# Performance work log

Measured on AMD Instinct MI355X. Metric: run time of the kernel, lower is better.

## Reference

```python
import jax, jax.numpy as jnp
import numpy as np

L, N, E = 2048, 2, 512
H = 8
HD = E // H
FF = 2048
NLAYERS = 2
EPS = 1e-5


def setup_inputs() -> dict:
    key = jax.random.key(0)
    ks = jax.random.split(key, 8)
    s = 0.02
    return {
        "src": jax.random.normal(ks[0], (L, N, E), jnp.float32),
        # packed qkv projection, torch Linear convention: y = x @ W.T + b
        "in_proj_w": jax.random.normal(ks[1], (NLAYERS, 3 * E, E), jnp.float32) * s,
        "in_proj_b": jnp.zeros((NLAYERS, 3 * E), jnp.float32),
        "out_proj_w": jax.random.normal(ks[2], (NLAYERS, E, E), jnp.float32) * s,
        "out_proj_b": jnp.zeros((NLAYERS, E), jnp.float32),
        "lin1_w": jax.random.normal(ks[3], (NLAYERS, FF, E), jnp.float32) * s,
        "lin1_b": jnp.zeros((NLAYERS, FF), jnp.float32),
        "lin2_w": jax.random.normal(ks[4], (NLAYERS, E, FF), jnp.float32) * s,
        "lin2_b": jnp.zeros((NLAYERS, E), jnp.float32),
        "ln1_g": jnp.ones((NLAYERS, E), jnp.float32),
        "ln1_b": jnp.zeros((NLAYERS, E), jnp.float32),
        "ln2_g": jnp.ones((NLAYERS, E), jnp.float32),
        "ln2_b": jnp.zeros((NLAYERS, E), jnp.float32),
    }


def _layer_norm(x, g, b):
    mu = jnp.mean(x, axis=-1, keepdims=True)
    var = jnp.mean(jnp.square(x - mu), axis=-1, keepdims=True)
    return (x - mu) * jax.lax.rsqrt(var + EPS) * g + b


def _mha(x, w_qkv, b_qkv, w_o, b_o):
    # x: [L, N, E] (seq-first, as in torch multi_head_attention_forward)
    qkv = jnp.einsum('lne,fe->lnf', x, w_qkv) + b_qkv  # [L, N, 3E]
    q, k, v = jnp.split(qkv, 3, axis=-1)
    q = q.reshape(L, N, H, HD) * (1.0 / np.sqrt(HD))  # torch scales q pre-bmm
    k = k.reshape(L, N, H, HD)
    v = v.reshape(L, N, H, HD)
    scores = jnp.einsum('lnhd,snhd->nhls', q, k)  # [N, H, L, S] -- O(L*S) matrix
    attn = jax.nn.softmax(scores, axis=-1)
    o = jnp.einsum('nhls,snhd->lnhd', attn, v).reshape(L, N, E)
    return jnp.einsum('lne,fe->lnf', o, w_o) + b_o


def reference(src, in_proj_w, in_proj_b, out_proj_w, out_proj_b,
              lin1_w, lin1_b, lin2_w, lin2_b, ln1_g, ln1_b, ln2_g, ln2_b):
    x = src
    for i in range(NLAYERS):  # fixed small layer count
        a = _mha(x, in_proj_w[i], in_proj_b[i], out_proj_w[i], out_proj_b[i])
        x = _layer_norm(x + a, ln1_g[i], ln1_b[i])  # post-norm (torch default)
        h = jax.nn.relu(jnp.einsum('lne,fe->lnf', x, lin1_w[i]) + lin1_b[i])
        f = jnp.einsum('lnf,ef->lne', h, lin2_w[i]) + lin2_b[i]
        x = _layer_norm(x + f, ln2_g[i], ln2_b[i])
    return x
```

## Files before the change

### kernel.cpp

```cpp
#include <hip/hip_runtime.h>
#include <hip/hip_bf16.h>

using bf16 = __hip_bfloat16;
typedef __bf16 bf16x8 __attribute__((ext_vector_type(8)));
typedef float f32x4 __attribute__((ext_vector_type(4)));

#define MFMA(a, b, c) __builtin_amdgcn_mfma_f32_16x16x32_bf16(a, b, c, 0, 0, 0)

constexpr int L = 2048, N = 2, E = 512, H = 8, HD = 64, FF = 2048;
constexpr int T = L * N;

__global__ void detect_dtype(const unsigned int* __restrict__ g,
                             int* __restrict__ flag) {
  if (threadIdx.x == 0 && blockIdx.x == 0)
    *flag = (g[0] != 0x3F800000u) ? 1 : 0;
}

__global__ __launch_bounds__(256) void cvt_to_bf16(
    const void* __restrict__ in, bf16* __restrict__ out, int n,
    const int* __restrict__ flag) {
  int i = (blockIdx.x * 256 + threadIdx.x) * 8;
  if (i >= n) return;
  if (*flag) {
    *(uint4*)&out[i] = *(const uint4*)&((const bf16*)in)[i];
  } else {
    float4 a = *(const float4*)&((const float*)in)[i];
    float4 b = *(const float4*)&((const float*)in)[i + 4];
    bf16 o8[8] = {__float2bfloat16(a.x), __float2bfloat16(a.y),
                  __float2bfloat16(a.z), __float2bfloat16(a.w),
                  __float2bfloat16(b.x), __float2bfloat16(b.y),
                  __float2bfloat16(b.z), __float2bfloat16(b.w)};
    *(uint4*)&out[i] = *(const uint4*)o8;
  }
}

__global__ __launch_bounds__(256) void cvt_to_f32(
    const void* __restrict__ in, float* __restrict__ out, int n,
    const int* __restrict__ flag) {
  int i = blockIdx.x * 256 + threadIdx.x;
  if (i >= n) return;
  out[i] = (*flag) ? __bfloat162float(((const bf16*)in)[i])
                   : ((const float*)in)[i];
}

__device__ __forceinline__ void gload16(const bf16* g, bf16* l) {
  __builtin_amdgcn_global_load_lds(
      (const __attribute__((address_space(1))) unsigned int*)g,
      (__attribute__((address_space(3))) unsigned int*)l, 16, 0, 0);
}

template <bool RELU>
__global__ __launch_bounds__(256) void gemm128(
    const bf16* __restrict__ A, const bf16* __restrict__ W,
    const float* __restrict__ bias, bf16* __restrict__ C,
    int M, int F, int K) {
  __shared__ __align__(16) bf16 As[2][128 * 32];
  __shared__ __align__(16) bf16 Bs[2][128 * 32];
  const int bm = blockIdx.x, bn = blockIdx.y;
  const int tid = threadIdx.x;
  const int w = tid >> 6, lane = tid & 63;
  const int wr = w >> 1, wc = w & 1;
  const int lhi = lane >> 4, llo = lane & 15;
  f32x4 acc[4][4] = {};

  const bf16 *ap[2], *wp[2];
#pragma unroll
  for (int s = 0; s < 2; ++s) {
    int c = tid + s * 256;
    ap[s] = &A[(size_t)(bm * 128 + (c >> 2)) * K + (c & 3) * 8];
    wp[s] = &W[(size_t)(bn * 128 + (c >> 2)) * K + (c & 3) * 8];
  }
  auto stage = [&](int buf, int k0) {
#pragma unroll
    for (int s = 0; s < 2; ++s) {
      gload16(ap[s] + k0, &As[buf][(tid + s * 256) * 8]);
      gload16(wp[s] + k0, &Bs[buf][(tid + s * 256) * 8]);
    }
  };

  stage(0, 0);
  int cur = 0;
  for (int k0 = 0; k0 < K; k0 += 32) {
    __syncthreads();
    if (k0 + 32 < K) stage(cur ^ 1, k0 + 32);
    bf16x8 af[4], bfr[4];
#pragma unroll
    for (int mi = 0; mi < 4; ++mi)
      af[mi] =
          *(const bf16x8*)&As[cur][(wr * 64 + mi * 16 + llo) * 32 + lhi * 8];
#pragma unroll
    for (int ni = 0; ni < 4; ++ni)
      bfr[ni] =
          *(const bf16x8*)&Bs[cur][(wc * 64 + ni * 16 + llo) * 32 + lhi * 8];
#pragma unroll
    for (int mi = 0; mi < 4; ++mi)
#pragma unroll
      for (int ni = 0; ni < 4; ++ni)
        acc[mi][ni] = MFMA(af[mi], bfr[ni], acc[mi][ni]);
    cur ^= 1;
  }
#pragma unroll
  for (int mi = 0; mi < 4; ++mi) {
#pragma unroll
    for (int ni = 0; ni < 4; ++ni) {
      int col = bn * 128 + wc * 64 + ni * 16 + llo;
      float bv = bias[col];
#pragma unroll
      for (int r = 0; r < 4; ++r) {
        int row = bm * 128 + wr * 64 + mi * 16 + lhi * 4 + r;
        float v = acc[mi][ni][r] + bv;
        if (RELU) v = fmaxf(v, 0.f);
        C[(size_t)row * F + col] = __float2bfloat16(v);
      }
    }
  }
}

template <bool RELU>
__global__ __launch_bounds__(256) void gemm64(
    const bf16* __restrict__ A, const bf16* __restrict__ W,
    const float* __restrict__ bias, bf16* __restrict__ C,
    int M, int F, int K) {
  __shared__ __align__(16) bf16 As[2][64 * 32];
  __shared__ __align__(16) bf16 Bs[2][64 * 32];
  const int bm = blockIdx.x, bn = blockIdx.y;
  const int tid = threadIdx.x;
  const int w = tid >> 6, lane = tid & 63;
  const int wr = w >> 1, wc = w & 1;
  const int lhi = lane >> 4, llo = lane & 15;
  f32x4 acc[2][2] = {};

  const bf16* ap = &A[(size_t)(bm * 64 + (tid >> 2)) * K + (tid & 3) * 8];
  const bf16* wp = &W[(size_t)(bn * 64 + (tid >> 2)) * K + (tid & 3) * 8];
  auto stage = [&](int buf, int k0) {
    gload16(ap + k0, &As[buf][tid * 8]);
    gload16(wp + k0, &Bs[buf][tid * 8]);
  };

  stage(0, 0);
  int cur = 0;
  for (int k0 = 0; k0 < K; k0 += 32) {
    __syncthreads();
    if (k0 + 32 < K) stage(cur ^ 1, k0 + 32);
    bf16x8 af[2], bfr[2];
#pragma unroll
    for (int mi = 0; mi < 2; ++mi)
      af[mi] =
          *(const bf16x8*)&As[cur][(wr * 32 + mi * 16 + llo) * 32 + lhi * 8];
#pragma unroll
    for (int ni = 0; ni < 2; ++ni)
      bfr[ni] =
          *(const bf16x8*)&Bs[cur][(wc * 32 + ni * 16 + llo) * 32 + lhi * 8];
#pragma unroll
    for (int mi = 0; mi < 2; ++mi)
#pragma unroll
      for (int ni = 0; ni < 2; ++ni)
        acc[mi][ni] = MFMA(af[mi], bfr[ni], acc[mi][ni]);
    cur ^= 1;
  }
#pragma unroll
  for (int mi = 0; mi < 2; ++mi) {
#pragma unroll
    for (int ni = 0; ni < 2; ++ni) {
      int col = bn * 64 + wc * 32 + ni * 16 + llo;
      float bv = bias[col];
#pragma unroll
      for (int r = 0; r < 4; ++r) {
        int row = bm * 64 + wr * 32 + mi * 16 + lhi * 4 + r;
        float v = acc[mi][ni][r] + bv;
        if (RELU) v = fmaxf(v, 0.f);
        C[(size_t)row * F + col] = __float2bfloat16(v);
      }
    }
  }
}

__global__ __launch_bounds__(256) void prep_kv(
    const bf16* __restrict__ qkv, bf16* __restrict__ kt,
    bf16* __restrict__ vt) {
  __shared__ __align__(16) bf16 Vl[64 * 72];
  const int blk = blockIdx.x;
  const int kb = blk & 31, nh = blk >> 5;
  const int n = nh >> 3, h = nh & 7;
  const int tid = threadIdx.x;
  bf16* ko = kt + ((size_t)nh * 32 + kb) * 4096;
  bf16* vo = vt + ((size_t)nh * 32 + kb) * 4096;
#pragma unroll
  for (int s = 0; s < 2; ++s) {
    int c = tid + s * 256;
    int jj = c >> 3, g = c & 7;
    size_t t = (size_t)((kb * 64 + jj) * N + n);
    uint4 kk = *(const uint4*)&qkv[t * 1536 + 512 + h * 64 + g * 8];
    *(uint4*)&ko[jj * 64 + ((g ^ (jj & 7)) * 8)] = kk;
    uint4 vv = *(const uint4*)&qkv[t * 1536 + 1024 + h * 64 + g * 8];
    *(uint4*)&Vl[jj * 72 + g * 8] = vv;
  }
  __syncthreads();
#pragma unroll
  for (int s = 0; s < 2; ++s) {
    int c = tid + s * 256;
    int d = c >> 3, gsw = c & 7;
    int g = gsw ^ (d & 7);
    bf16 tmp[8];
#pragma unroll
    for (int e = 0; e < 8; ++e) tmp[e] = Vl[(g * 8 + e) * 72 + d];
    *(uint4*)&vo[d * 64 + gsw * 8] = *(const uint4*)tmp;
  }
}

__global__ __launch_bounds__(256) void attn_split(
    const bf16* __restrict__ qkv, const bf16* __restrict__ kt,
    const bf16* __restrict__ vt, float* __restrict__ opart,
    float* __restrict__ lpart) {
  __shared__ __align__(16) bf16 Kb[2][4096];
  __shared__ __align__(16) bf16 Vb[2][4096];
  __shared__ __align__(16) bf16 Ps[64 * 72];
  const int blk = blockIdx.x;
  const int qb = blk & 31;
  const int nh = (blk >> 5) & 15;
  const int split = blk >> 9;
  const int n = nh >> 3, h = nh & 7;
  const int tid = threadIdx.x;
  const int w = tid >> 6, lane = tid & 63;
  const int lhi = lane >> 4, llo = lane & 15;
  const int kb0 = split * 16, kb1 = kb0 + 16;

#pragma unroll
  for (int s = 0; s < 2; ++s) {
    int c = tid + s * 256;
    int i = c >> 3, dc = c & 7;
    size_t t = (size_t)((qb * 64 + i) * N + n);
    *(uint4*)&Ps[i * 72 + dc * 8] =
        *(const uint4*)&qkv[t * 1536 + h * 64 + dc * 8];
  }
  __syncthreads();
  bf16x8 aq[2];
  aq[0] = *(const bf16x8*)&Ps[(w * 16 + llo) * 72 + 0 + lhi * 8];
  aq[1] = *(const bf16x8*)&Ps[(w * 16 + llo) * 72 + 32 + lhi * 8];

  const bf16* ktile = kt + (size_t)nh * 32 * 4096;
  const bf16* vtile = vt + (size_t)nh * 32 * 4096;
  auto stage = [&](int buf, int kb) {
#pragma unroll
    for (int s = 0; s < 2; ++s) {
      int c = tid + s * 256;
      gload16(ktile + (size_t)kb * 4096 + c * 8, &Kb[buf][c * 8]);
      gload16(vtile + (size_t)kb * 4096 + c * 8, &Vb[buf][c * 8]);
    }
  };
  stage(0, kb0);

  float psum[4] = {0.f, 0.f, 0.f, 0.f};
  f32x4 o[4] = {};
  int cur = 0;

  for (int kb = kb0; kb < kb1; ++kb) {
    __syncthreads();
    if (kb + 1 < kb1) stage(cur ^ 1, kb + 1);

    f32x4 sfr[4] = {};
    __builtin_amdgcn_s_setprio(1);
#pragma unroll
    for (int cb = 0; cb < 4; ++cb) {
      const int row = cb * 16 + llo;
#pragma unroll
      for (int ks = 0; ks < 2; ++ks) {
        bf16x8 b = *(const bf16x8*)&Kb[cur]
            [row * 64 + (((ks * 4 + lhi) ^ (row & 7)) << 3)];
        sfr[cb] = MFMA(aq[ks], b, sfr[cb]);
      }
    }
    __builtin_amdgcn_s_setprio(0);

#pragma unroll
    for (int cb = 0; cb < 4; ++cb) {
#pragma unroll
      for (int r = 0; r < 4; ++r) {
        float p = __expf(sfr[cb][r] * 0.125f);
        psum[r] += p;
        Ps[(w * 16 + lhi * 4 + r) * 72 + cb * 16 + llo] = __float2bfloat16(p);
      }
    }
    asm volatile("" ::: "memory");

    __builtin_amdgcn_s_setprio(1);
#pragma unroll
    for (int cb = 0; cb < 4; ++cb) {
      const int crow = cb * 16 + llo;
#pragma unroll
      for (int ks = 0; ks < 2; ++ks) {
        bf16x8 a =
            *(const bf16x8*)&Ps[(w * 16 + llo) * 72 + ks * 32 + lhi * 8];
        bf16x8 b = *(const bf16x8*)&Vb[cur]
            [crow * 64 + (((ks * 4 + lhi) ^ (crow & 7)) << 3)];
        o[cb] = MFMA(a, b, o[cb]);
      }
    }
    __builtin_amdgcn_s_setprio(0);
    cur ^= 1;
  }

#pragma unroll
  for (int r = 0; r < 4; ++r) {
    float v = psum[r];
#pragma unroll
    for (int d = 1; d < 16; d <<= 1) v += __shfl_xor(v, d);
    psum[r] = v;
  }
#pragma unroll
  for (int cb = 0; cb < 4; ++cb) {
#pragma unroll
    for (int r = 0; r < 4; ++r) {
      int i = w * 16 + lhi * 4 + r;
      int d = cb * 16 + llo;
      size_t t = (size_t)((qb * 64 + i) * N + n);
      opart[((size_t)split * T + t) * E + h * 64 + d] = o[cb][r];
    }
  }
  if (llo == 0) {
#pragma unroll
    for (int r = 0; r < 4; ++r) {
      int i = w * 16 + lhi * 4 + r;
      size_t t = (size_t)((qb * 64 + i) * N + n);
      lpart[(size_t)(split * T + t) * H + h] = psum[r];
    }
  }
}

__global__ __launch_bounds__(256) void attn_merge(
    const float* __restrict__ opart, const float* __restrict__ lpart,
    bf16* __restrict__ atn) {
  int i = (blockIdx.x * 256 + threadIdx.x) * 4;
  if (i >= T * E) return;
  int t = i >> 9;
  int h = (i >> 6) & 7;
  float4 o0 = *(const float4*)&opart[i];
  float4 o1 = *(const float4*)&opart[(size_t)T * E + i];
  float rl = 1.f / (lpart[(size_t)t * H + h] + lpart[(size_t)(T + t) * H + h]);
  bf16 r4[4] = {__float2bfloat16((o0.x + o1.x) * rl),
                __float2bfloat16((o0.y + o1.y) * rl),
                __float2bfloat16((o0.z + o1.z) * rl),
                __float2bfloat16((o0.w + o1.w) * rl)};
  *(uint2*)&atn[i] = *(const uint2*)r4;
}

template <typename OutT>
__global__ __launch_bounds__(256) void add_ln(
    const bf16* __restrict__ res, const bf16* __restrict__ y,
    const float* __restrict__ g, const float* __restrict__ b,
    OutT* __restrict__ out) {
  const int t = blockIdx.x;
  const int tid = threadIdx.x;
  const int w = tid >> 6, lane = tid & 63;
  const int e = tid * 2;
  const size_t base = (size_t)t * E;
  float v0 = __bfloat162float(res[base + e]) + __bfloat162float(y[base + e]);
  float v1 = __bfloat162float(res[base + e + 1]) + __bfloat162float(y[base + e + 1]);
  float s = v0 + v1, q = v0 * v0 + v1 * v1;
#pragma unroll
  for (int d = 1; d < 64; d <<= 1) {
    s += __shfl_xor(s, d);
    q += __shfl_xor(q, d);
  }
  __shared__ float rs[4], rq[4];
  if (lane == 0) { rs[w] = s; rq[w] = q; }
  __syncthreads();
  float S = rs[0] + rs[1] + rs[2] + rs[3];
  float Qq = rq[0] + rq[1] + rq[2] + rq[3];
  float mu = S * (1.f / E);
  float var = Qq * (1.f / E) - mu * mu;
  float rstd = rsqrtf(var + 1e-5f);
  float o0 = (v0 - mu) * rstd * g[e] + b[e];
  float o1 = (v1 - mu) * rstd * g[e + 1] + b[e + 1];
  if constexpr (__is_same(OutT, float)) {
    out[base + e] = o0;
    out[base + e + 1] = o1;
  } else {
    out[base + e] = __float2bfloat16(o0);
    out[base + e + 1] = __float2bfloat16(o1);
  }
}

extern "C" void kernel_launch(void* const* d_in, const int* in_sizes, int n_in,
                              void* d_out, int out_size, void* d_ws,
                              size_t ws_size, hipStream_t stream) {
  int* flag = (int*)d_ws;
  float* pbuf = (float*)((char*)d_ws + 16);
  float* in_b = pbuf;
  float* ob   = in_b + 3072;
  float* l1b  = ob + 1024;
  float* l2b  = l1b + 4096;
  float* ln1g = l2b + 1024;
  float* ln1b = ln1g + 1024;
  float* ln2g = ln1b + 1024;
  float* ln2b = ln2g + 1024;
  bf16* big  = (bf16*)(ln2b + 1024);
  bf16* srcb = big;
  bf16* in_w = srcb + (size_t)T * E;
  bf16* ow   = in_w + (size_t)2 * 1536 * E;
  bf16* l1w  = ow + (size_t)2 * E * E;
  bf16* l2w  = l1w + (size_t)2 * FF * E;
  bf16* qkv  = l2w + (size_t)2 * E * FF;
  bf16* atn  = qkv + (size_t)T * 1536;
  bf16* ybuf = atn + (size_t)T * E;
  bf16* x1   = ybuf + (size_t)T * E;
  bf16* x2   = x1 + (size_t)T * E;
  bf16* hbuf = x2 + (size_t)T * E;
  bf16* ktg  = hbuf + (size_t)T * FF;
  bf16* vtg  = ktg + (size_t)T * E;
  float* opart = (float*)hbuf;
  float* lpart = (float*)ybuf;

  detect_dtype<<<1, 64, 0, stream>>>((const unsigned int*)d_in[9], flag);
  auto cvtb = [&](const void* in, bf16* out, int n) {
    cvt_to_bf16<<<dim3(n / 2048), 256, 0, stream>>>(in, out, n, flag);
  };
  auto cvtf = [&](const void* in, float* out, int n) {
    cvt_to_f32<<<dim3(n / 256), 256, 0, stream>>>(in, out, n, flag);
  };
  cvtb(d_in[0], srcb, T * E);
  cvtb(d_in[1], in_w, 2 * 1536 * E);
  cvtb(d_in[3], ow, 2 * E * E);
  cvtb(d_in[5], l1w, 2 * FF * E);
  cvtb(d_in[7], l2w, 2 * E * FF);
  cvtf(d_in[2], in_b, 3072);
  cvtf(d_in[4], ob, 1024);
  cvtf(d_in[6], l1b, 4096);
  cvtf(d_in[8], l2b, 1024);
  cvtf(d_in[9], ln1g, 1024);
  cvtf(d_in[10], ln1b, 1024);
  cvtf(d_in[11], ln2g, 1024);
  cvtf(d_in[12], ln2b, 1024);

  const bf16* x = srcb;
  for (int i = 0; i < 2; ++i) {
    gemm128<false><<<dim3(T / 128, 1536 / 128), 256, 0, stream>>>(
        x, in_w + (size_t)i * 1536 * E, in_b + i * 1536, qkv, T, 1536, E);
    prep_kv<<<dim3(512), 256, 0, stream>>>(qkv, ktg, vtg);
    attn_split<<<dim3(1024), 256, 0, stream>>>(qkv, ktg, vtg, opart, lpart);
    attn_merge<<<dim3(T * E / 1024), 256, 0, stream>>>(opart, lpart, atn);
    gemm64<false><<<dim3(T / 64, E / 64), 256, 0, stream>>>(
        atn, ow + (size_t)i * E * E, ob + i * E, ybuf, T, E, E);
    add_ln<bf16><<<dim3(T), 256, 0, stream>>>(
        x, ybuf, ln1g + i * E, ln1b + i * E, x1);
    gemm128<true><<<dim3(T / 128, FF / 128), 256, 0, stream>>>(
        x1, l1w + (size_t)i * FF * E, l1b + i * FF, hbuf, T, FF, E);
    gemm64<false><<<dim3(T / 64, E / 64), 256, 0, stream>>>(
        hbuf, l2w + (size_t)i * E * FF, l2b + i * E, ybuf, T, E, FF);
    if (i == 1) {
      add_ln<float><<<dim3(T), 256, 0, stream>>>(
          x1, ybuf, ln2g + i * E, ln2b + i * E, (float*)d_out);
    } else {
      add_ln<bf16><<<dim3(T), 256, 0, stream>>>(
          x1, ybuf, ln2g + i * E, ln2b + i * E, x2);
    }
    x = x2;
  }
}
```

Before: 326.4 us.

## Deepen GEMM pipeline to four stages and split attention four ways with bf16 partials

```diff
diff --git a/kernel.cpp b/kernel.cpp
--- a/kernel.cpp
+++ b/kernel.cpp
@@ -49,124 +49,94 @@
       (__attribute__((address_space(3))) unsigned int*)l, 16, 0, 0);
 }
 
-template <bool RELU>
-__global__ __launch_bounds__(256) void gemm128(
+template <bool RELU, int BN>
+__global__ __launch_bounds__(256) void gemm_pipe(
     const bf16* __restrict__ A, const bf16* __restrict__ W,
     const float* __restrict__ bias, bf16* __restrict__ C,
     int M, int F, int K) {
-  __shared__ __align__(16) bf16 As[2][128 * 32];
-  __shared__ __align__(16) bf16 Bs[2][128 * 32];
+  constexpr int D = 4;
+  constexpr int GB = BN / 64;
+  constexpr int FN = BN / 32;
+  __shared__ __align__(16) bf16 As[D][128 * 32];
+  __shared__ __align__(16) bf16 Bs[D][BN * 32];
   const int bm = blockIdx.x, bn = blockIdx.y;
   const int tid = threadIdx.x;
   const int w = tid >> 6, lane = tid & 63;
   const int wr = w >> 1, wc = w & 1;
   const int lhi = lane >> 4, llo = lane & 15;
-  f32x4 acc[4][4] = {};
-
-  const bf16 *ap[2], *wp[2];
+  f32x4 acc[4][FN] = {};
+
+  const bf16 *ap[2], *wp[GB];
 #pragma unroll
   for (int s = 0; s < 2; ++s) {
     int c = tid + s * 256;
     ap[s] = &A[(size_t)(bm * 128 + (c >> 2)) * K + (c & 3) * 8];
-    wp[s] = &W[(size_t)(bn * 128 + (c >> 2)) * K + (c & 3) * 8];
+  }
+#pragma unroll
+  for (int s = 0; s < GB; ++s) {
+    int c = tid + s * 256;
+    wp[s] = &W[(size_t)(bn * BN + (c >> 2)) * K + (c & 3) * 8];
   }
   auto stage = [&](int buf, int k0) {
 #pragma unroll
-    for (int s = 0; s < 2; ++s) {
+    for (int s = 0; s < 2; ++s)
       gload16(ap[s] + k0, &As[buf][(tid + s * 256) * 8]);
+#pragma unroll
+    for (int s = 0; s < GB; ++s)
       gload16(wp[s] + k0, &Bs[buf][(tid + s * 256) * 8]);
-    }
   };
 
+  const int nsteps = K / 32;
   stage(0, 0);
-  int cur = 0;
-  for (int k0 = 0; k0 < K; k0 += 32) {
-    __syncthreads();
-    if (k0 + 32 < K) stage(cur ^ 1, k0 + 32);
-    bf16x8 af[4], bfr[4];
+  stage(1, 32);
+  stage(2, 64);
+
+  for (int t = 0; t < nsteps; ++t) {
+    const int cur = t & 3;
+    if (t < nsteps - 2) {
+      if constexpr (BN == 128)
+        asm volatile("s_waitcnt vmcnt(8)" ::: "memory");
+      else
+        asm volatile("s_waitcnt vmcnt(6)" ::: "memory");
+    } else if (t == nsteps - 2) {
+      if constexpr (BN == 128)
+        asm volatile("s_waitcnt vmcnt(4)" ::: "memory");
+      else
+        asm volatile("s_waitcnt vmcnt(3)" ::: "memory");
+    } else {
+      asm volatile("s_waitcnt vmcnt(0)" ::: "memory");
+    }
+    __builtin_amdgcn_s_barrier();
+    asm volatile("" ::: "memory");
+    __builtin_amdgcn_sched_barrier(0);
+    if (t + 3 < nsteps) stage((t + 3) & 3, (t + 3) * 32);
+
+    bf16x8 af[4], bfr[FN];
 #pragma unroll
     for (int mi = 0; mi < 4; ++mi)
       af[mi] =
           *(const bf16x8*)&As[cur][(wr * 64 + mi * 16 + llo) * 32 + lhi * 8];
 #pragma unroll
-    for (int ni = 0; ni < 4; ++ni)
-      bfr[ni] =
-          *(const bf16x8*)&Bs[cur][(wc * 64 + ni * 16 + llo) * 32 + lhi * 8];
+    for (int ni = 0; ni < FN; ++ni)
+      bfr[ni] = *(const bf16x8*)&Bs[cur]
+          [(wc * (FN * 16) + ni * 16 + llo) * 32 + lhi * 8];
+    __builtin_amdgcn_s_setprio(1);
 #pragma unroll
     for (int mi = 0; mi < 4; ++mi)
 #pragma unroll
-      for (int ni = 0; ni < 4; ++ni)
+      for (int ni = 0; ni < FN; ++ni)
         acc[mi][ni] = MFMA(af[mi], bfr[ni], acc[mi][ni]);
-    cur ^= 1;
+    __builtin_amdgcn_s_setprio(0);
   }
 #pragma unroll
   for (int mi = 0; mi < 4; ++mi) {
 #pragma unroll
-    for (int ni = 0; ni < 4; ++ni) {
-      int col = bn * 128 + wc * 64 + ni * 16 + llo;
+    for (int ni = 0; ni < FN; ++ni) {
+      int col = bn * BN + wc * (FN * 16) + ni * 16 + llo;
       float bv = bias[col];
 #pragma unroll
       for (int r = 0; r < 4; ++r) {
         int row = bm * 128 + wr * 64 + mi * 16 + lhi * 4 + r;
-        float v = acc[mi][ni][r] + bv;
-        if (RELU) v = fmaxf(v, 0.f);
-        C[(size_t)row * F + col] = __float2bfloat16(v);
-      }
-    }
-  }
-}
-
-template <bool RELU>
-__global__ __launch_bounds__(256) void gemm64(
-    const bf16* __restrict__ A, const bf16* __restrict__ W,
-    const float* __restrict__ bias, bf16* __restrict__ C,
-    int M, int F, int K) {
-  __shared__ __align__(16) bf16 As[2][64 * 32];
-  __shared__ __align__(16) bf16 Bs[2][64 * 32];
-  const int bm = blockIdx.x, bn = blockIdx.y;
-  const int tid = threadIdx.x;
-  const int w = tid >> 6, lane = tid & 63;
-  const int wr = w >> 1, wc = w & 1;
-  const int lhi = lane >> 4, llo = lane & 15;
-  f32x4 acc[2][2] = {};
-
-  const bf16* ap = &A[(size_t)(bm * 64 + (tid >> 2)) * K + (tid & 3) * 8];
-  const bf16* wp = &W[(size_t)(bn * 64 + (tid >> 2)) * K + (tid & 3) * 8];
-  auto stage = [&](int buf, int k0) {
-    gload16(ap + k0, &As[buf][tid * 8]);
-    gload16(wp + k0, &Bs[buf][tid * 8]);
-  };
-
-  stage(0, 0);
-  int cur = 0;
-  for (int k0 = 0; k0 < K; k0 += 32) {
-    __syncthreads();
-    if (k0 + 32 < K) stage(cur ^ 1, k0 + 32);
-    bf16x8 af[2], bfr[2];
-#pragma unroll
-    for (int mi = 0; mi < 2; ++mi)
-      af[mi] =
-          *(const bf16x8*)&As[cur][(wr * 32 + mi * 16 + llo) * 32 + lhi * 8];
-#pragma unroll
-    for (int ni = 0; ni < 2; ++ni)
-      bfr[ni] =
-          *(const bf16x8*)&Bs[cur][(wc * 32 + ni * 16 + llo) * 32 + lhi * 8];
-#pragma unroll
-    for (int mi = 0; mi < 2; ++mi)
-#pragma unroll
-      for (int ni = 0; ni < 2; ++ni)
-        acc[mi][ni] = MFMA(af[mi], bfr[ni], acc[mi][ni]);
-    cur ^= 1;
-  }
-#pragma unroll
-  for (int mi = 0; mi < 2; ++mi) {
-#pragma unroll
-    for (int ni = 0; ni < 2; ++ni) {
-      int col = bn * 64 + wc * 32 + ni * 16 + llo;
-      float bv = bias[col];
-#pragma unroll
-      for (int r = 0; r < 4; ++r) {
-        int row = bm * 64 + wr * 32 + mi * 16 + lhi * 4 + r;
         float v = acc[mi][ni][r] + bv;
         if (RELU) v = fmaxf(v, 0.f);
         C[(size_t)row * F + col] = __float2bfloat16(v);
@@ -210,7 +180,7 @@
 
 __global__ __launch_bounds__(256) void attn_split(
     const bf16* __restrict__ qkv, const bf16* __restrict__ kt,
-    const bf16* __restrict__ vt, float* __restrict__ opart,
+    const bf16* __restrict__ vt, bf16* __restrict__ opart,
     float* __restrict__ lpart) {
   __shared__ __align__(16) bf16 Kb[2][4096];
   __shared__ __align__(16) bf16 Vb[2][4096];
@@ -223,7 +193,7 @@
   const int tid = threadIdx.x;
   const int w = tid >> 6, lane = tid & 63;
   const int lhi = lane >> 4, llo = lane & 15;
-  const int kb0 = split * 16, kb1 = kb0 + 16;
+  const int kb0 = split * 8, kb1 = kb0 + 8;
 
 #pragma unroll
   for (int s = 0; s < 2; ++s) {
@@ -314,7 +284,8 @@
       int i = w * 16 + lhi * 4 + r;
       int d = cb * 16 + llo;
       size_t t = (size_t)((qb * 64 + i) * N + n);
-      opart[((size_t)split * T + t) * E + h * 64 + d] = o[cb][r];
+      opart[((size_t)split * T + t) * E + h * 64 + d] =
+          __float2bfloat16(o[cb][r]);
     }
   }
   if (llo == 0) {
@@ -328,20 +299,25 @@
 }
 
 __global__ __launch_bounds__(256) void attn_merge(
-    const float* __restrict__ opart, const float* __restrict__ lpart,
+    const bf16* __restrict__ opart, const float* __restrict__ lpart,
     bf16* __restrict__ atn) {
-  int i = (blockIdx.x * 256 + threadIdx.x) * 4;
+  int i = (blockIdx.x * 256 + threadIdx.x) * 8;
   if (i >= T * E) return;
-  int t = i >> 9;
-  int h = (i >> 6) & 7;
-  float4 o0 = *(const float4*)&opart[i];
-  float4 o1 = *(const float4*)&opart[(size_t)T * E + i];
-  float rl = 1.f / (lpart[(size_t)t * H + h] + lpart[(size_t)(T + t) * H + h]);
-  bf16 r4[4] = {__float2bfloat16((o0.x + o1.x) * rl),
-                __float2bfloat16((o0.y + o1.y) * rl),
-                __float2bfloat16((o0.z + o1.z) * rl),
-                __float2bfloat16((o0.w + o1.w) * rl)};
-  *(uint2*)&atn[i] = *(const uint2*)r4;
+  int t = i >> 9, h = (i >> 6) & 7;
+  float l = 0.f, acc[8] = {};
+#pragma unroll
+  for (int s = 0; s < 4; ++s) {
+    l += lpart[(size_t)(s * T + t) * H + h];
+    uint4 v = *(const uint4*)&opart[(size_t)s * T * E + i];
+    const bf16* e8 = (const bf16*)&v;
+#pragma unroll
+    for (int e = 0; e < 8; ++e) acc[e] += __bfloat162float(e8[e]);
+  }
+  float rl = 1.f / l;
+  bf16 r8[8];
+#pragma unroll
+  for (int e = 0; e < 8; ++e) r8[e] = __float2bfloat16(acc[e] * rl);
+  *(uint4*)&atn[i] = *(const uint4*)r8;
 }
 
 template <typename OutT>
@@ -408,7 +384,7 @@
   bf16* hbuf = x2 + (size_t)T * E;
   bf16* ktg  = hbuf + (size_t)T * FF;
   bf16* vtg  = ktg + (size_t)T * E;
-  float* opart = (float*)hbuf;
+  bf16* opart  = hbuf;
   float* lpart = (float*)ybuf;
 
   detect_dtype<<<1, 64, 0, stream>>>((const unsigned int*)d_in[9], flag);
@@ -434,18 +410,18 @@
 
   const bf16* x = srcb;
   for (int i = 0; i < 2; ++i) {
-    gemm128<false><<<dim3(T / 128, 1536 / 128), 256, 0, stream>>>(
+    gemm_pipe<false, 128><<<dim3(T / 128, 1536 / 128), 256, 0, stream>>>(
         x, in_w + (size_t)i * 1536 * E, in_b + i * 1536, qkv, T, 1536, E);
     prep_kv<<<dim3(512), 256, 0, stream>>>(qkv, ktg, vtg);
-    attn_split<<<dim3(1024), 256, 0, stream>>>(qkv, ktg, vtg, opart, lpart);
-    attn_merge<<<dim3(T * E / 1024), 256, 0, stream>>>(opart, lpart, atn);
-    gemm64<false><<<dim3(T / 64, E / 64), 256, 0, stream>>>(
+    attn_split<<<dim3(2048), 256, 0, stream>>>(qkv, ktg, vtg, opart, lpart);
+    attn_merge<<<dim3(T * E / 2048), 256, 0, stream>>>(opart, lpart, atn);
+    gemm_pipe<false, 64><<<dim3(T / 128, E / 64), 256, 0, stream>>>(
         atn, ow + (size_t)i * E * E, ob + i * E, ybuf, T, E, E);
     add_ln<bf16><<<dim3(T), 256, 0, stream>>>(
         x, ybuf, ln1g + i * E, ln1b + i * E, x1);
-    gemm128<true><<<dim3(T / 128, FF / 128), 256, 0, stream>>>(
+    gemm_pipe<true, 128><<<dim3(T / 128, FF / 128), 256, 0, stream>>>(
         x1, l1w + (size_t)i * FF * E, l1b + i * FF, hbuf, T, FF, E);
-    gemm64<false><<<dim3(T / 64, E / 64), 256, 0, stream>>>(
+    gemm_pipe<false, 64><<<dim3(T / 128, E / 64), 256, 0, stream>>>(
         hbuf, l2w + (size_t)i * E * FF, l2b + i * E, ybuf, T, E, FF);
     if (i == 1) {
       add_ln<float><<<dim3(T), 256, 0, stream>>>(
```

New measurement: 337.6 us. 1.03x slower.
